# Kernel tuning notes

Hardware: AMD Instinct MI355X
Metric: run time of the kernel (lower is better)

## Reference

```python
import jax, jax.numpy as jnp
import numpy as np

# Filter.__init__ constants: fs=200000, nfft=20000, fc=42000, f_low=30000, f_high=60000
FS = 200000.0
NFFT = 20000
FC = 42000.0
F_LOW = 30000.0
F_HIGH = 60000.0
_f_full = np.linspace(0.0, FS / 2, NFFT // 2 + 1)
F_BAND = _f_full[(_f_full > F_LOW) & (_f_full < F_HIGH)]          # (2999,) in-band freqs
FC_INDEX = int(np.argmin(np.abs(F_BAND - FC)))                    # index of fc in band (1199)
NOISE_MASK = np.asarray((F_BAND < 40000.0) | (F_BAND > 44000.0))  # static bool freq mask


def setup_inputs() -> dict:
    key = jax.random.key(0)
    # x: (B0, B1, C, F, T) -- STFT stack; C=2 (real/imag-like channels), F=len(F_BAND)
    x = jax.random.normal(key, (8, 4, 2, F_BAND.shape[0], 400), dtype=jnp.float32)
    return {"x": x}


def reference(x):
    B0, B1, C, F, T = x.shape
    spec = x.reshape(-1, C, F, T)                      # (N, C, F, T)
    mag = jnp.sum(jnp.abs(spec), axis=1)               # (N, F, T)
    mid = jnp.argmax(mag[:, FC_INDEX, :], axis=1)      # (N,) pulse center per item

    t = jnp.arange(T)
    # windowed sum over time [mid-20, mid+20) (left clamp at 0 is automatic since t>=0)
    pw = ((t[None, :] >= mid[:, None] - 20) & (t[None, :] < mid[:, None] + 20)).astype(mag.dtype)
    pulse = jnp.einsum('nft,nt->nf', mag, pw)          # (N, F)

    noise = jnp.mean(mag[:, jnp.asarray(NOISE_MASK), :], axis=(1, 2))   # (N,)
    sig = pulse[:, FC_INDEX]                                            # (N,)
    snr = 10.0 * jnp.log10((sig - noise) ** 2 / noise ** 2)
    # int() in torch truncates toward zero -> jnp.trunc
    hb = jnp.maximum(jnp.trunc(6.0 * (snr - 48.0) + 27.0).astype(jnp.int32), 8)  # (N,)

    fidx = jnp.arange(F)
    fmask = (fidx[None, :] >= FC_INDEX - hb[:, None]) & (fidx[None, :] < FC_INDEX + hb[:, None])  # (N, F)
    tmask = (t[None, :] >= mid[:, None] - 8) & (t[None, :] < mid[:, None] + 8)                    # (N, T)
    # original loop assigns filtered[:, :, fslice, tslice] for EVERY i -> union of all windows
    keep = jnp.any(fmask[:, :, None] & tmask[:, None, :], axis=0)      # (F, T)

    out = spec * keep[None, None, :, :].astype(spec.dtype)             # (N, C, F, T)
    return out.reshape(x.shape)
```

## Files before the change

### kernel.cpp

```cpp
#include <hip/hip_runtime.h>
#include <math.h>

#define N_BATCH 32
#define NF 2999
#define NT 400
#define NT4 100
#define FC_IDX 1199
#define NOISE_LO 999
#define NOISE_HI 1400
#define NOISE_F 2598
#define NOISE_CNT (NOISE_F * NT)
#define PLANE4 (NF * NT4)

__global__ void kA_fcrow(const float* __restrict__ x, int* __restrict__ mid_out,
                         float* __restrict__ sig_out, float* __restrict__ noise_sum) {
    const int n = blockIdx.x;
    const int tid = threadIdx.x;
    __shared__ float mag[NT];
    __shared__ float rv[256];
    __shared__ int   ri[256];

    const float* p0 = x + ((size_t)(n * 2 + 0) * NF + FC_IDX) * NT;
    const float* p1 = x + ((size_t)(n * 2 + 1) * NF + FC_IDX) * NT;
    for (int t = tid; t < NT; t += 256)
        mag[t] = fabsf(p0[t]) + fabsf(p1[t]);
    __syncthreads();

    float bv = -1.0f; int bi = NT;
    for (int t = tid; t < NT; t += 256) {
        float v = mag[t];
        if (v > bv) { bv = v; bi = t; }
    }
    rv[tid] = bv; ri[tid] = bi;
    __syncthreads();
    for (int s = 128; s > 0; s >>= 1) {
        if (tid < s) {
            float v2 = rv[tid + s]; int i2 = ri[tid + s];
            if (v2 > rv[tid] || (v2 == rv[tid] && i2 < ri[tid])) { rv[tid] = v2; ri[tid] = i2; }
        }
        __syncthreads();
    }
    if (tid == 0) {
        const int mid = ri[0];
        int lo = mid - 20; if (lo < 0) lo = 0;
        int hi = mid + 20; if (hi > NT) hi = NT;
        float s = 0.0f;
        for (int t = lo; t < hi; ++t) s += mag[t];
        mid_out[n]   = mid;
        sig_out[n]   = s;
        noise_sum[n] = 0.0f;
    }
}

__global__ void kB_noise(const float* __restrict__ x, float* __restrict__ noise_sum) {
    const int n = blockIdx.y;
    const int per_n = 2 * NOISE_F * NT4;
    const size_t base = (size_t)n * 2 * PLANE4;
    const float4* __restrict__ x4 = (const float4*)x;

    float part = 0.0f;
    for (int i = blockIdx.x * 256 + threadIdx.x; i < per_n; i += gridDim.x * 256) {
        int c   = i / (NOISE_F * NT4);
        int rem = i - c * (NOISE_F * NT4);
        int fj  = rem / NT4;
        int t4  = rem - fj * NT4;
        int f   = (fj < NOISE_LO) ? fj : fj + (NOISE_HI - NOISE_LO);
        float4 v = x4[base + (size_t)(c * NF + f) * NT4 + t4];
        part += fabsf(v.x) + fabsf(v.y) + fabsf(v.z) + fabsf(v.w);
    }
    for (int off = 32; off > 0; off >>= 1) part += __shfl_down(part, off, 64);
    __shared__ float ws[4];
    const int lane = threadIdx.x & 63, wv = threadIdx.x >> 6;
    if (lane == 0) ws[wv] = part;
    __syncthreads();
    if (threadIdx.x == 0)
        atomicAdd(&noise_sum[n], ws[0] + ws[1] + ws[2] + ws[3]);
}

__global__ void kC_masks(const int* __restrict__ mid_in, const float* __restrict__ sig_in,
                         const float* __restrict__ noise_sum,
                         unsigned* __restrict__ Fm, unsigned* __restrict__ Tm) {
    __shared__ int s_hb[N_BATCH];
    __shared__ int s_mid[N_BATCH];
    const int tid = threadIdx.x;
    if (tid < N_BATCH) {
        float noise = noise_sum[tid] / (float)NOISE_CNT;
        float d = sig_in[tid] - noise;
        float snr = 10.0f * log10f((d * d) / (noise * noise));
        int hb = (int)truncf(6.0f * (snr - 48.0f) + 27.0f);
        if (hb < 8) hb = 8;
        s_hb[tid]  = hb;
        s_mid[tid] = mid_in[tid];
    }
    __syncthreads();
    for (int f = tid; f < NF; f += 256) {
        unsigned w = 0;
        #pragma unroll
        for (int n = 0; n < N_BATCH; ++n)
            if (f >= FC_IDX - s_hb[n] && f < FC_IDX + s_hb[n]) w |= 1u << n;
        Fm[f] = w;
    }
    for (int t = tid; t < NT; t += 256) {
        unsigned w = 0;
        #pragma unroll
        for (int n = 0; n < N_BATCH; ++n)
            if (t >= s_mid[n] - 8 && t < s_mid[n] + 8) w |= 1u << n;
        Tm[t] = w;
    }
}

__global__ void kD_write(const float* __restrict__ x, float* __restrict__ out,
                         const unsigned* __restrict__ Fm, const unsigned* __restrict__ Tm) {
    const int nc = blockIdx.y;
    const int i  = blockIdx.x * 256 + threadIdx.x;
    if (i >= PLANE4) return;
    const int f  = i / NT4;
    const int t4 = (i - f * NT4) * 4;
    const size_t idx = (size_t)nc * PLANE4 + i;
    float4 r = make_float4(0.f, 0.f, 0.f, 0.f);
    const unsigned fm = Fm[f];
    if (fm != 0) {
        float4 v = ((const float4*)x)[idx];
        if (fm & Tm[t4 + 0]) r.x = v.x;
        if (fm & Tm[t4 + 1]) r.y = v.y;
        if (fm & Tm[t4 + 2]) r.z = v.z;
        if (fm & Tm[t4 + 3]) r.w = v.w;
    }
    ((float4*)out)[idx] = r;
}

extern "C" void kernel_launch(void* const* d_in, const int* in_sizes, int n_in,
                              void* d_out, int out_size, void* d_ws, size_t ws_size,
                              hipStream_t stream) {
    const float* x = (const float*)d_in[0];
    float* out = (float*)d_out;

    char* ws = (char*)d_ws;
    int*      mid   = (int*)(ws + 0);
    float*    sig   = (float*)(ws + 128);
    float*    noise = (float*)(ws + 256);
    unsigned* Fm    = (unsigned*)(ws + 384);
    unsigned* Tm    = (unsigned*)(ws + 384 + NF * 4);

    kA_fcrow<<<N_BATCH, 256, 0, stream>>>(x, mid, sig, noise);
    kB_noise<<<dim3(128, N_BATCH), 256, 0, stream>>>(x, noise);
    kC_masks<<<1, 256, 0, stream>>>(mid, sig, noise, Fm, Tm);
    kD_write<<<dim3((PLANE4 + 255) / 256, 64), 256, 0, stream>>>(x, out, Fm, Tm);
}
```

Before: 520.2 us.

## Merge fc-row and noise kernels, replace atomics with partials, vectorize mask writes

Folds the argmax/pulse kernel and the noise-sum kernel into one launch, using extra blocks per batch item. Noise partial sums are now written per block and reduced in the mask kernel, so the atomicAdd and the zero-init dependency go away. The write kernel handles two float4s per thread and loads the time mask as a uint4. It also drops the per-element division in the noise indexing loop. This saves one launch, but the write kernel dominates and is memory-bound, so the benefit is small.

```diff
diff --git a/kernel.cpp b/kernel.cpp
--- a/kernel.cpp
+++ b/kernel.cpp
@@ -11,85 +11,93 @@
 #define NOISE_F 2598
 #define NOISE_CNT (NOISE_F * NT)
 #define PLANE4 (NF * NT4)
+#define NOISE_BLOCKS 128
+#define SPAN_C (NOISE_F * NT4)
+#define SPAN1 (NOISE_LO * NT4)
+#define GAP   ((NOISE_HI - NOISE_LO) * NT4)
 
-__global__ void kA_fcrow(const float* __restrict__ x, int* __restrict__ mid_out,
-                         float* __restrict__ sig_out, float* __restrict__ noise_sum) {
-    const int n = blockIdx.x;
+__global__ void k1_stats(const float* __restrict__ x, float* __restrict__ partials,
+                         int* __restrict__ mid_out, float* __restrict__ sig_out) {
+    const int n = blockIdx.y;
     const int tid = threadIdx.x;
     __shared__ float mag[NT];
     __shared__ float rv[256];
     __shared__ int   ri[256];
 
-    const float* p0 = x + ((size_t)(n * 2 + 0) * NF + FC_IDX) * NT;
-    const float* p1 = x + ((size_t)(n * 2 + 1) * NF + FC_IDX) * NT;
-    for (int t = tid; t < NT; t += 256)
-        mag[t] = fabsf(p0[t]) + fabsf(p1[t]);
-    __syncthreads();
-
-    float bv = -1.0f; int bi = NT;
-    for (int t = tid; t < NT; t += 256) {
-        float v = mag[t];
-        if (v > bv) { bv = v; bi = t; }
-    }
-    rv[tid] = bv; ri[tid] = bi;
-    __syncthreads();
-    for (int s = 128; s > 0; s >>= 1) {
-        if (tid < s) {
-            float v2 = rv[tid + s]; int i2 = ri[tid + s];
-            if (v2 > rv[tid] || (v2 == rv[tid] && i2 < ri[tid])) { rv[tid] = v2; ri[tid] = i2; }
+    if (blockIdx.x < NOISE_BLOCKS) {
+        const float4* __restrict__ x4 = (const float4*)x;
+        const size_t base = (size_t)n * 2 * PLANE4;
+        float part = 0.0f;
+        const int stride = NOISE_BLOCKS * 256;
+        for (int j = blockIdx.x * 256 + tid; j < 2 * SPAN_C; j += stride) {
+            const int c   = (j >= SPAN_C) ? 1 : 0;
+            const int k   = j - (c ? SPAN_C : 0);
+            const int off = (k < SPAN1) ? k : k + GAP;
+            const float4 v = x4[base + (size_t)c * PLANE4 + off];
+            part += fabsf(v.x) + fabsf(v.y) + fabsf(v.z) + fabsf(v.w);
         }
+        for (int o = 32; o > 0; o >>= 1) part += __shfl_down(part, o, 64);
+        if ((tid & 63) == 0) rv[tid >> 6] = part;
         __syncthreads();
-    }
-    if (tid == 0) {
-        const int mid = ri[0];
-        int lo = mid - 20; if (lo < 0) lo = 0;
-        int hi = mid + 20; if (hi > NT) hi = NT;
-        float s = 0.0f;
-        for (int t = lo; t < hi; ++t) s += mag[t];
-        mid_out[n]   = mid;
-        sig_out[n]   = s;
-        noise_sum[n] = 0.0f;
+        if (tid == 0)
+            partials[n * NOISE_BLOCKS + blockIdx.x] = rv[0] + rv[1] + rv[2] + rv[3];
+    } else {
+        const float* p0 = x + ((size_t)(n * 2 + 0) * NF + FC_IDX) * NT;
+        const float* p1 = x + ((size_t)(n * 2 + 1) * NF + FC_IDX) * NT;
+        for (int t = tid; t < NT; t += 256)
+            mag[t] = fabsf(p0[t]) + fabsf(p1[t]);
+        __syncthreads();
+        float bv = -1.0f; int bi = NT;
+        for (int t = tid; t < NT; t += 256) {
+            float v = mag[t];
+            if (v > bv) { bv = v; bi = t; }
+        }
+        rv[tid] = bv; ri[tid] = bi;
+        __syncthreads();
+        for (int s = 128; s > 0; s >>= 1) {
+            if (tid < s) {
+                float v2 = rv[tid + s]; int i2 = ri[tid + s];
+                if (v2 > rv[tid] || (v2 == rv[tid] && i2 < ri[tid])) { rv[tid] = v2; ri[tid] = i2; }
+            }
+            __syncthreads();
+        }
+        if (tid == 0) {
+            const int mid = ri[0];
+            int lo = mid - 20; if (lo < 0) lo = 0;
+            int hi = mid + 20; if (hi > NT) hi = NT;
+            float s = 0.0f;
+            for (int t = lo; t < hi; ++t) s += mag[t];
+            mid_out[n] = mid;
+            sig_out[n] = s;
+        }
     }
 }
 
-__global__ void kB_noise(const float* __restrict__ x, float* __restrict__ noise_sum) {
-    const int n = blockIdx.y;
-    const int per_n = 2 * NOISE_F * NT4;
-    const size_t base = (size_t)n * 2 * PLANE4;
-    const float4* __restrict__ x4 = (const float4*)x;
-
-    float part = 0.0f;
-    for (int i = blockIdx.x * 256 + threadIdx.x; i < per_n; i += gridDim.x * 256) {
-        int c   = i / (NOISE_F * NT4);
-        int rem = i - c * (NOISE_F * NT4);
-        int fj  = rem / NT4;
-        int t4  = rem - fj * NT4;
-        int f   = (fj < NOISE_LO) ? fj : fj + (NOISE_HI - NOISE_LO);
-        float4 v = x4[base + (size_t)(c * NF + f) * NT4 + t4];
-        part += fabsf(v.x) + fabsf(v.y) + fabsf(v.z) + fabsf(v.w);
-    }
-    for (int off = 32; off > 0; off >>= 1) part += __shfl_down(part, off, 64);
-    __shared__ float ws[4];
-    const int lane = threadIdx.x & 63, wv = threadIdx.x >> 6;
-    if (lane == 0) ws[wv] = part;
-    __syncthreads();
-    if (threadIdx.x == 0)
-        atomicAdd(&noise_sum[n], ws[0] + ws[1] + ws[2] + ws[3]);
-}
-
-__global__ void kC_masks(const int* __restrict__ mid_in, const float* __restrict__ sig_in,
-                         const float* __restrict__ noise_sum,
+__global__ void k2_masks(const float* __restrict__ partials, const int* __restrict__ mid_in,
+                         const float* __restrict__ sig_in,
                          unsigned* __restrict__ Fm, unsigned* __restrict__ Tm) {
+    __shared__ float s[256];
     __shared__ int s_hb[N_BATCH];
     __shared__ int s_mid[N_BATCH];
     const int tid = threadIdx.x;
+    const float4* p4 = (const float4*)partials;
+    float acc = 0.0f;
+    #pragma unroll
+    for (int q = 0; q < 4; ++q) {
+        float4 v = p4[tid * 4 + q];
+        acc += v.x + v.y + v.z + v.w;
+    }
+    s[tid] = acc;
+    __syncthreads();
     if (tid < N_BATCH) {
-        float noise = noise_sum[tid] / (float)NOISE_CNT;
+        float ns = 0.0f;
+        #pragma unroll
+        for (int q = 0; q < 8; ++q) ns += s[tid * 8 + q];
+        float noise = ns / (float)NOISE_CNT;
         float d = sig_in[tid] - noise;
         float snr = 10.0f * log10f((d * d) / (noise * noise));
         int hb = (int)truncf(6.0f * (snr - 48.0f) + 27.0f);
-        if (hb < 8) hb = 8;
-        s_hb[tid]  = hb;
+        s_hb[tid]  = hb < 8 ? 8 : hb;
         s_mid[tid] = mid_in[tid];
     }
     __syncthreads();
@@ -109,24 +117,29 @@
     }
 }
 
-__global__ void kD_write(const float* __restrict__ x, float* __restrict__ out,
+__global__ void k3_write(const float* __restrict__ x, float* __restrict__ out,
                          const unsigned* __restrict__ Fm, const unsigned* __restrict__ Tm) {
     const int nc = blockIdx.y;
-    const int i  = blockIdx.x * 256 + threadIdx.x;
-    if (i >= PLANE4) return;
-    const int f  = i / NT4;
-    const int t4 = (i - f * NT4) * 4;
-    const size_t idx = (size_t)nc * PLANE4 + i;
-    float4 r = make_float4(0.f, 0.f, 0.f, 0.f);
-    const unsigned fm = Fm[f];
-    if (fm != 0) {
-        float4 v = ((const float4*)x)[idx];
-        if (fm & Tm[t4 + 0]) r.x = v.x;
-        if (fm & Tm[t4 + 1]) r.y = v.y;
-        if (fm & Tm[t4 + 2]) r.z = v.z;
-        if (fm & Tm[t4 + 3]) r.w = v.w;
+    const size_t pbase = (size_t)nc * PLANE4;
+    int i = blockIdx.x * 512 + threadIdx.x;
+    #pragma unroll
+    for (int r = 0; r < 2; ++r, i += 256) {
+        if (i < PLANE4) {
+            const int f  = i / NT4;
+            const int t4 = (i - f * NT4) * 4;
+            float4 rv = make_float4(0.f, 0.f, 0.f, 0.f);
+            const unsigned fm = Fm[f];
+            if (fm != 0) {
+                const float4 v = ((const float4*)x)[pbase + i];
+                const uint4 tm = *(const uint4*)(Tm + t4);
+                if (fm & tm.x) rv.x = v.x;
+                if (fm & tm.y) rv.y = v.y;
+                if (fm & tm.z) rv.z = v.z;
+                if (fm & tm.w) rv.w = v.w;
+            }
+            ((float4*)out)[pbase + i] = rv;
+        }
     }
-    ((float4*)out)[idx] = r;
 }
 
 extern "C" void kernel_launch(void* const* d_in, const int* in_sizes, int n_in,
@@ -136,14 +149,13 @@
     float* out = (float*)d_out;
 
     char* ws = (char*)d_ws;
-    int*      mid   = (int*)(ws + 0);
-    float*    sig   = (float*)(ws + 128);
-    float*    noise = (float*)(ws + 256);
-    unsigned* Fm    = (unsigned*)(ws + 384);
-    unsigned* Tm    = (unsigned*)(ws + 384 + NF * 4);
+    float*    partials = (float*)(ws + 0);
+    int*      mid      = (int*)(ws + 16384);
+    float*    sig      = (float*)(ws + 16512);
+    unsigned* Fm       = (unsigned*)(ws + 16640);
+    unsigned* Tm       = (unsigned*)(ws + 28640);
 
-    kA_fcrow<<<N_BATCH, 256, 0, stream>>>(x, mid, sig, noise);
-    kB_noise<<<dim3(128, N_BATCH), 256, 0, stream>>>(x, noise);
-    kC_masks<<<1, 256, 0, stream>>>(mid, sig, noise, Fm, Tm);
-    kD_write<<<dim3((PLANE4 + 255) / 256, 64), 256, 0, stream>>>(x, out, Fm, Tm);
+    k1_stats<<<dim3(NOISE_BLOCKS + 1, N_BATCH), 256, 0, stream>>>(x, partials, mid, sig);
+    k2_masks<<<1, 256, 0, stream>>>(partials, mid, sig, Fm, Tm);
+    k3_write<<<dim3((PLANE4 + 511) / 512, 64), 256, 0, stream>>>(x, out, Fm, Tm);
 }
```

After: 486.4 us. 1.07x faster.
